# Kernel tuning notes

Measured on AMD Instinct MI355X. Metric: run time of the kernel, lower is better.

## Reference

```python
import jax, jax.numpy as jnp
import numpy as np

D_MODEL = 2048
FFN_MULT = 4
N_ROUTED = 8
TOP_K = 2
H_ROUTED = FFN_MULT * D_MODEL // N_ROUTED   # 1024
H_SHARED = FFN_MULT * D_MODEL               # 8192


def setup_inputs() -> dict:
    key = jax.random.key(0)
    ks = jax.random.split(key, 8)
    s = 0.02
    x = jax.random.normal(ks[0], (4, 2048, D_MODEL), dtype=jnp.float32)
    w_gate = jax.random.normal(ks[1], (N_ROUTED, D_MODEL), dtype=jnp.float32) * s
    Wg = jax.random.normal(ks[2], (N_ROUTED, D_MODEL, H_ROUTED), dtype=jnp.float32) * s
    Wu = jax.random.normal(ks[3], (N_ROUTED, D_MODEL, H_ROUTED), dtype=jnp.float32) * s
    Wd = jax.random.normal(ks[4], (N_ROUTED, H_ROUTED, D_MODEL), dtype=jnp.float32) * s
    Sg = jax.random.normal(ks[5], (D_MODEL, H_SHARED), dtype=jnp.float32) * s
    Su = jax.random.normal(ks[6], (D_MODEL, H_SHARED), dtype=jnp.float32) * s
    Sd = jax.random.normal(ks[7], (H_SHARED, D_MODEL), dtype=jnp.float32) * s
    return {"x": x, "w_gate": w_gate, "Wg": Wg, "Wu": Wu, "Wd": Wd,
            "Sg": Sg, "Su": Su, "Sd": Sd}


def reference(x, w_gate, Wg, Wu, Wd, Sg, Su, Sd):
    B, T, D = x.shape
    N = B * T
    xf = x.reshape(N, D)

    # shared expert (n_shared = 1)
    shared = (jax.nn.silu(xf @ Sg) * (xf @ Su)) @ Sd          # [N, D]

    # gate (eval mode: clean logits, no noise)
    clean = xf @ w_gate.T                                      # [N, E]
    top_logits, top_idx = jax.lax.top_k(clean, TOP_K)          # [N, K]
    gates = jax.nn.softmax(top_logits, axis=-1)                # [N, K]
    # load-balance loss
    importance = jax.nn.softmax(clean, axis=-1).sum(0)         # [E]
    ce = importance / N * N_ROUTED
    lb_loss = jnp.mean(ce * ce)

    # combine weights: combine[n,e] = sum_k gates[n,k] * (top_idx[n,k]==e)
    onehot = jax.nn.one_hot(top_idx, N_ROUTED, dtype=xf.dtype)  # [N, K, E]
    combine = jnp.einsum('nke,nk->ne', onehot, gates)           # [N, E]

    # routed experts (dense grouped form, zero-weight tokens contribute 0)
    hg = jnp.einsum('nd,edh->neh', xf, Wg)
    hu = jnp.einsum('nd,edh->neh', xf, Wu)
    h = jax.nn.silu(hg) * hu                                    # [N, E, H]
    routed = jnp.einsum('neh,ehd,ne->nd', h, Wd, combine)       # [N, D]

    out = (shared + routed).reshape(B, T, D)
    return out, lb_loss
```

## Files before the change

### kernel.cpp

```cpp
#include <hip/hip_runtime.h>
#include <hip/hip_bf16.h>
#include <hip/hip_fp16.h>
#include <stdint.h>

#define NTOK   8192
#define DM     2048
#define NEXP   8
#define HR     1024
#define HS     8192
#define ROWS_MAX 18432

typedef _Float16 f16;
typedef f16  f16x8 __attribute__((ext_vector_type(8)));
typedef float f32x4 __attribute__((ext_vector_type(4)));

#define GLP(p) ((const __attribute__((address_space(1))) void*)(p))
#define LDP(p) ((__attribute__((address_space(3))) void*)(p))

static __device__ __forceinline__ float silu_f(float v) {
  return v / (1.0f + __expf(-v));
}

static __device__ __forceinline__ int xcd_swz(int bid, int nwg) {
  const int q = nwg >> 3, r = nwg & 7;
  const int x = bid & 7, i = bid >> 3;
  return (x < r ? x * (q + 1) : r * (q + 1) + (x - r) * q) + i;
}


__global__ __launch_bounds__(256)
void conv_x_kernel(const float* __restrict__ in, f16* __restrict__ out, int n8) {
  const int i = blockIdx.x * 256 + threadIdx.x;
  if (i >= n8) return;
  const float4* p = (const float4*)in + (size_t)i * 2;
  const float4 a = p[0], b = p[1];
  f16x8 o;
  o[0] = (f16)a.x; o[1] = (f16)a.y; o[2] = (f16)a.z; o[3] = (f16)a.w;
  o[4] = (f16)b.x; o[5] = (f16)b.y; o[6] = (f16)b.z; o[7] = (f16)b.w;
  ((f16x8*)out)[i] = o;
}

__global__ __launch_bounds__(256)
void conv_t_kernel(const float* __restrict__ in, f16* __restrict__ out,
                   int R, int C, size_t ostride) {
  __shared__ float t[32][33];
  const int b = blockIdx.z;
  const float* inb = in + (size_t)b * R * C;
  f16* outb = out + (size_t)b * ostride;
  const int c0 = blockIdx.x * 32, r0 = blockIdx.y * 32;
  const int tx = threadIdx.x, ty0 = threadIdx.y;
#pragma unroll
  for (int yy = 0; yy < 4; ++yy) {
    const int ty = ty0 + yy * 8;
    t[ty][tx] = inb[(size_t)(r0 + ty) * C + (c0 + tx)];
  }
  __syncthreads();
#pragma unroll
  for (int yy = 0; yy < 4; ++yy) {
    const int ty = ty0 + yy * 8;
    outb[(size_t)(c0 + ty) * R + (r0 + tx)] = (f16)t[tx][ty];
  }
}


__global__ __launch_bounds__(256)
void gate_kernel(const float* __restrict__ x, const float* __restrict__ wgate,
                 float* __restrict__ gateW, int* __restrict__ gateI,
                 float* __restrict__ importance, int* __restrict__ cnt) {
  __shared__ float impl[NEXP];
  __shared__ int cntl[NEXP];
  const int tid = threadIdx.x, lane = tid & 63, wid = tid >> 6;
  if (tid < NEXP) { impl[tid] = 0.f; cntl[tid] = 0; }
  __syncthreads();
  for (int s = 0; s < 8; ++s) {
    const int t = blockIdx.x * 32 + wid * 8 + s;
    const float* xr = x + (size_t)t * DM;
    float pv[NEXP] = {0.f, 0.f, 0.f, 0.f, 0.f, 0.f, 0.f, 0.f};
    for (int j = 0; j < DM / 64; ++j) {
      const int c = lane + j * 64;
      const float xv = xr[c];
#pragma unroll
      for (int e = 0; e < NEXP; ++e) pv[e] += xv * wgate[e * DM + c];
    }
#pragma unroll
    for (int e = 0; e < NEXP; ++e) {
#pragma unroll
      for (int st = 32; st >= 1; st >>= 1) pv[e] += __shfl_xor(pv[e], st);
    }
    if (lane == 0) {
      float v1 = pv[0]; int i1 = 0;
#pragma unroll
      for (int e = 1; e < NEXP; ++e) if (pv[e] > v1) { v1 = pv[e]; i1 = e; }
      float v2 = -1e30f; int i2 = 0;
#pragma unroll
      for (int e = 0; e < NEXP; ++e) if (e != i1 && pv[e] > v2) { v2 = pv[e]; i2 = e; }
      const float g1 = 1.f / (1.f + expf(v2 - v1));
      gateW[t * 2 + 0] = g1;  gateW[t * 2 + 1] = 1.f - g1;
      gateI[t * 2 + 0] = i1;  gateI[t * 2 + 1] = i2;
      float mx = pv[0];
#pragma unroll
      for (int e = 1; e < NEXP; ++e) mx = fmaxf(mx, pv[e]);
      float sum = 0.f, ex[NEXP];
#pragma unroll
      for (int e = 0; e < NEXP; ++e) { ex[e] = expf(pv[e] - mx); sum += ex[e]; }
      const float inv = 1.f / sum;
#pragma unroll
      for (int e = 0; e < NEXP; ++e) atomicAdd(&impl[e], ex[e] * inv);
      atomicAdd(&cntl[i1], 1);
      atomicAdd(&cntl[i2], 1);
    }
  }
  __syncthreads();
  if (tid < NEXP) {
    atomicAdd(&importance[tid], impl[tid]);
    atomicAdd(&cnt[tid], cntl[tid]);
  }
}

__global__ void scan_kernel(const int* __restrict__ cnt, int* __restrict__ seg,
                            int* __restrict__ cursor, const float* __restrict__ imp,
                            float* __restrict__ lb_out) {
  if (threadIdx.x == 0 && blockIdx.x == 0) {
    int o = 0;
#pragma unroll
    for (int e = 0; e < NEXP; ++e) {
      seg[e] = o;
      o += (cnt[e] + 255) & ~255;
      cursor[e] = 0;
    }
    seg[NEXP] = o;
    float s = 0.f;
#pragma unroll
    for (int e = 0; e < NEXP; ++e) {
      const float ce = imp[e] * ((float)NEXP / (float)NTOK);
      s += ce * ce;
    }
    *lb_out = s / (float)NEXP;
  }
}

__global__ __launch_bounds__(256)
void scatter_kernel(const float* __restrict__ gateW, const int* __restrict__ gateI,
                    const int* __restrict__ seg, int* __restrict__ cursor,
                    int* __restrict__ rowtok, float* __restrict__ rowgate) {
  const int t = blockIdx.x * 256 + threadIdx.x;
  const int lane = threadIdx.x & 63;
#pragma unroll
  for (int k = 0; k < 2; ++k) {
    const int e = gateI[t * 2 + k];
    const float g = gateW[t * 2 + k];
    for (int ee = 0; ee < NEXP; ++ee) {
      const unsigned long long m = __ballot(e == ee);
      if (e == ee) {
        const int leader = __ffsll((unsigned long long)m) - 1;
        const int rank = (int)__popcll(m & ((1ull << lane) - 1ull));
        int base = 0;
        if (lane == leader) base = atomicAdd(&cursor[ee], (int)__popcll(m));
        base = __shfl(base, leader);
        const int pos = seg[ee] + base + rank;
        rowtok[pos] = t;
        rowgate[pos] = g;
      }
    }
  }
}


struct G8Ptrs { const f16* a[4]; const f16* b[4]; };

static __device__ __forceinline__ void swz_rc(int tid, int i, int& r, int& c) {
  const int L = i * 8192 + tid * 16;
  const int U = L ^ (((L >> 7) & 7) << 4);
  r = U >> 7;
  c = (U & 127) >> 1;
}

static __device__ __forceinline__ void stage8(const G8Ptrs& P, int koff,
                                              f16* AsB, f16* BsB, int wid) {
#pragma unroll
  for (int i = 0; i < 4; ++i) {
    __builtin_amdgcn_global_load_lds(GLP(P.a[i] + koff), LDP(AsB + i * 4096 + wid * 512), 16, 0, 0);
    __builtin_amdgcn_global_load_lds(GLP(P.b[i] + koff), LDP(BsB + i * 4096 + wid * 512), 16, 0, 0);
  }
}

static __device__ __forceinline__ void g8_mainloop(const G8Ptrs& P, int nt,
                                                   f16* As, f16* Bs,
                                                   f32x4 (&acc)[8][4]) {
  const int tid = threadIdx.x;
  const int lane = tid & 63, wid = tid >> 6;
  const int wr = wid >> 2, wc = wid & 3;
  const int fr = lane & 15, fk = (lane >> 4) * 8;

  stage8(P, 0, As, Bs, wid);
  asm volatile("s_waitcnt vmcnt(0)" ::: "memory");
  __syncthreads();

  for (int t = 0; t < nt; ++t) {
    const int cur = t & 1;
    if (t + 1 < nt)
      stage8(P, (t + 1) * 64, As + (cur ^ 1) * 16384, Bs + (cur ^ 1) * 16384, wid);
    const f16* Ab = As + cur * 16384;
    const f16* Bb = Bs + cur * 16384;
    f16x8 bf[4][2];
#pragma unroll
    for (int n = 0; n < 4; ++n) {
      const int r = wc * 64 + n * 16 + fr;
      const int sw = (r & 7) << 3;
#pragma unroll
      for (int ks = 0; ks < 2; ++ks)
        bf[n][ks] = *(const f16x8*)&Bb[(r * 64 + ks * 32 + fk) ^ sw];
    }
#pragma unroll
    for (int mh = 0; mh < 2; ++mh) {
#pragma unroll
      for (int ks = 0; ks < 2; ++ks) {
        f16x8 af[4];
#pragma unroll
        for (int m = 0; m < 4; ++m) {
          const int r = wr * 128 + (mh * 4 + m) * 16 + fr;
          af[m] = *(const f16x8*)&Ab[(r * 64 + ks * 32 + fk) ^ ((r & 7) << 3)];
        }
#pragma unroll
        for (int m = 0; m < 4; ++m)
#pragma unroll
          for (int n = 0; n < 4; ++n)
            acc[mh * 4 + m][n] =
                __builtin_amdgcn_mfma_f32_16x16x32_f16(af[m], bf[n][ks], acc[mh * 4 + m][n], 0, 0, 0);
      }
    }
    asm volatile("s_waitcnt vmcnt(0)" ::: "memory");
    __syncthreads();
  }
}

__global__ __launch_bounds__(512, 2)
void g8_gu(const f16* __restrict__ A, const f16* __restrict__ B,
           f16* __restrict__ C, int gx, int N, int K) {
  __shared__ f16 As[2 * 16384], Bs[2 * 16384];
  const int lin = xcd_swz(blockIdx.x, gridDim.x);
  const int row0 = (lin % gx) * 256, n0 = (lin / gx) * 256;
  const int tid = threadIdx.x;
  G8Ptrs P;
#pragma unroll
  for (int i = 0; i < 4; ++i) {
    int r, c; swz_rc(tid, i, r, c);
    P.a[i] = A + (size_t)(row0 + r) * K + c;
    P.b[i] = B + (size_t)(n0 + r) * K + c;
  }
  f32x4 acc[8][4] = {};
  g8_mainloop(P, K / 64, As, Bs, acc);
  const int lane = tid & 63, wid = tid >> 6;
  const int wr = wid >> 2, wc = wid & 3;
  const int fr = lane & 15, r0 = (lane >> 4) * 4;
#pragma unroll
  for (int m = 0; m < 8; ++m)
#pragma unroll
    for (int n = 0; n < 4; ++n)
#pragma unroll
      for (int rr = 0; rr < 4; ++rr) {
        const int row = row0 + wr * 128 + m * 16 + r0 + rr;
        const int col = n0 + wc * 64 + n * 16 + fr;
        C[(size_t)row * N + col] = (f16)acc[m][n][rr];
      }
}

__global__ __launch_bounds__(512, 2)
void g8_down(const f16* __restrict__ A, const f16* __restrict__ B,
             float* __restrict__ out, int gx, int N, int K, int kchunk) {
  __shared__ f16 As[2 * 16384], Bs[2 * 16384];
  const int lin = xcd_swz(blockIdx.x, gridDim.x);
  const int row0 = (lin % gx) * 256, n0 = (lin / gx) * 256;
  const int k0 = blockIdx.y * kchunk;
  const int tid = threadIdx.x;
  G8Ptrs P;
#pragma unroll
  for (int i = 0; i < 4; ++i) {
    int r, c; swz_rc(tid, i, r, c);
    P.a[i] = A + (size_t)(row0 + r) * K + k0 + c;
    P.b[i] = B + (size_t)(n0 + r) * K + k0 + c;
  }
  f32x4 acc[8][4] = {};
  g8_mainloop(P, kchunk / 64, As, Bs, acc);
  const int lane = tid & 63, wid = tid >> 6;
  const int wr = wid >> 2, wc = wid & 3;
  const int fr = lane & 15, r0 = (lane >> 4) * 4;
#pragma unroll
  for (int m = 0; m < 8; ++m)
#pragma unroll
    for (int n = 0; n < 4; ++n)
#pragma unroll
      for (int rr = 0; rr < 4; ++rr) {
        const int row = row0 + wr * 128 + m * 16 + r0 + rr;
        const int col = n0 + wc * 64 + n * 16 + fr;
        atomicAdd(&out[(size_t)row * N + col], acc[m][n][rr]);
      }
}

__global__ __launch_bounds__(512, 2)
void g8_rgu(const f16* __restrict__ x16, const int* __restrict__ rowtok,
            const f16* __restrict__ Wgu, f16* __restrict__ C,
            const int* __restrict__ seg) {
  __shared__ f16 As[2 * 16384], Bs[2 * 16384];
  const int e = blockIdx.z;
  const int row0 = seg[e] + blockIdx.y * 256;
  if (row0 >= seg[e + 1]) return;
  const int n0 = blockIdx.x * 256;
  const f16* Bbase = Wgu + (size_t)e * 2048 * DM;
  const int tid = threadIdx.x;
  G8Ptrs P;
#pragma unroll
  for (int i = 0; i < 4; ++i) {
    int r, c; swz_rc(tid, i, r, c);
    int tok = rowtok[row0 + r];
    if (tok < 0) tok = 0;
    P.a[i] = x16 + (size_t)tok * DM + c;
    P.b[i] = Bbase + (size_t)(n0 + r) * DM + c;
  }
  f32x4 acc[8][4] = {};
  g8_mainloop(P, DM / 64, As, Bs, acc);
  const int lane = tid & 63, wid = tid >> 6;
  const int wr = wid >> 2, wc = wid & 3;
  const int fr = lane & 15, r0 = (lane >> 4) * 4;
#pragma unroll
  for (int m = 0; m < 8; ++m)
#pragma unroll
    for (int n = 0; n < 4; ++n)
#pragma unroll
      for (int rr = 0; rr < 4; ++rr) {
        const int row = row0 + wr * 128 + m * 16 + r0 + rr;
        const int col = n0 + wc * 64 + n * 16 + fr;
        C[(size_t)row * 2048 + col] = (f16)acc[m][n][rr];
      }
}

__global__ __launch_bounds__(512, 2)
void g8_rdown(const f16* __restrict__ A, const f16* __restrict__ B,
              float* __restrict__ out, const int* __restrict__ seg,
              const int* __restrict__ rowtok, const float* __restrict__ rowgate) {
  __shared__ f16 As[2 * 16384], Bs[2 * 16384];
  const int e = blockIdx.z;
  const int row0 = seg[e] + blockIdx.y * 256;
  if (row0 >= seg[e + 1]) return;
  const int n0 = blockIdx.x * 256;
  const f16* Bbase = B + (size_t)e * DM * HR;
  const int tid = threadIdx.x;
  G8Ptrs P;
#pragma unroll
  for (int i = 0; i < 4; ++i) {
    int r, c; swz_rc(tid, i, r, c);
    P.a[i] = A + (size_t)(row0 + r) * HR + c;
    P.b[i] = Bbase + (size_t)(n0 + r) * HR + c;
  }
  f32x4 acc[8][4] = {};
  g8_mainloop(P, HR / 64, As, Bs, acc);
  const int lane = tid & 63, wid = tid >> 6;
  const int wr = wid >> 2, wc = wid & 3;
  const int fr = lane & 15, r0 = (lane >> 4) * 4;
#pragma unroll
  for (int m = 0; m < 8; ++m)
#pragma unroll
    for (int rr = 0; rr < 4; ++rr) {
      const int pos = row0 + wr * 128 + m * 16 + r0 + rr;
      const int tok = rowtok[pos];
      if (tok >= 0) {
        const float gw = rowgate[pos];
#pragma unroll
        for (int n = 0; n < 4; ++n) {
          const int col = n0 + wc * 64 + n * 16 + fr;
          atomicAdd(&out[(size_t)tok * DM + col], acc[m][n][rr] * gw);
        }
      }
    }
}


__global__ __launch_bounds__(256)
void silu_shared_kernel(const f16* __restrict__ gu, f16* __restrict__ h) {
  const int idx = blockIdx.x * 256 + threadIdx.x;
  const int r = idx >> 10, c8 = idx & 1023;
  const f16x8 g8 = ((const f16x8*)(gu + (size_t)r * 16384))[c8];
  const f16x8 u8 = ((const f16x8*)(gu + (size_t)r * 16384 + 8192))[c8];
  f16x8 o;
#pragma unroll
  for (int j = 0; j < 8; ++j)
    o[j] = (f16)(silu_f((float)g8[j]) * (float)u8[j]);
  ((f16x8*)(h + (size_t)r * 8192))[c8] = o;
}

__global__ __launch_bounds__(256)
void silu_routed_kernel(const f16* __restrict__ gu, f16* __restrict__ hr) {
  const int idx = blockIdx.x * 256 + threadIdx.x;
  const int r = idx >> 7, c8 = idx & 127;
  const f16x8 g8 = ((const f16x8*)(gu + (size_t)r * 2048))[c8];
  const f16x8 u8 = ((const f16x8*)(gu + (size_t)r * 2048 + 1024))[c8];
  f16x8 o;
#pragma unroll
  for (int j = 0; j < 8; ++j)
    o[j] = (f16)(silu_f((float)g8[j]) * (float)u8[j]);
  ((f16x8*)(hr + (size_t)r * 1024))[c8] = o;
}


extern "C" void kernel_launch(void* const* d_in, const int* in_sizes, int n_in,
                              void* d_out, int out_size, void* d_ws, size_t ws_size,
                              hipStream_t stream) {
  const float* x  = (const float*)d_in[0];
  const float* wg = (const float*)d_in[1];
  const float* Wg = (const float*)d_in[2];
  const float* Wu = (const float*)d_in[3];
  const float* Wd = (const float*)d_in[4];
  const float* Sg = (const float*)d_in[5];
  const float* Su = (const float*)d_in[6];
  const float* Sd = (const float*)d_in[7];
  float* out = (float*)d_out;

  char* p = (char*)d_ws;
  auto take = [&](size_t b) { char* q = p; p += (b + 255) & ~(size_t)255; return q; };
  float* importance = (float*)take(32);
  int*   cnt        = (int*)take(32);
  int*   cursor     = (int*)take(32);
  int*   seg        = (int*)take(64);
  int*   rowtok     = (int*)take((size_t)ROWS_MAX * 4);
  float* rowgate    = (float*)take((size_t)ROWS_MAX * 4);
  float* gateW      = (float*)take((size_t)NTOK * 2 * 4);
  int*   gateI      = (int*)take((size_t)NTOK * 2 * 4);
  f16* x16   = (f16*)take((size_t)NTOK * DM * 2);
  f16* SguT  = (f16*)take((size_t)2 * HS * DM * 2);
  f16* SdT   = (f16*)take((size_t)DM * HS * 2);
  f16* WguT  = (f16*)take((size_t)NEXP * 2048 * DM * 2);
  f16* WdT   = (f16*)take((size_t)NEXP * DM * HR * 2);
  f16* hbuf  = (f16*)take((size_t)4096 * HS * 2);
  f16* hr    = (f16*)take((size_t)ROWS_MAX * HR * 2);
  f16* gubuf = (f16*)take((size_t)ROWS_MAX * 2048 * 2);
  if ((size_t)(p - (char*)d_ws) > ws_size) return;

  hipMemsetAsync(out, 0, (size_t)out_size * 4, stream);
  hipMemsetAsync(importance, 0, 768, stream);
  hipMemsetAsync(rowtok, 0xFF, (size_t)ROWS_MAX * 4, stream);

  conv_x_kernel<<<(NTOK * DM / 8 + 255) / 256, 256, 0, stream>>>(x, x16, NTOK * DM / 8);
  dim3 tb(32, 8);
  conv_t_kernel<<<dim3(HS / 32, DM / 32, 1), tb, 0, stream>>>(Sg, SguT, DM, HS, 0);
  conv_t_kernel<<<dim3(HS / 32, DM / 32, 1), tb, 0, stream>>>(Su, SguT + (size_t)HS * DM, DM, HS, 0);
  conv_t_kernel<<<dim3(DM / 32, HS / 32, 1), tb, 0, stream>>>(Sd, SdT, HS, DM, 0);
  conv_t_kernel<<<dim3(HR / 32, DM / 32, NEXP), tb, 0, stream>>>(Wg, WguT, DM, HR, (size_t)2048 * DM);
  conv_t_kernel<<<dim3(HR / 32, DM / 32, NEXP), tb, 0, stream>>>(Wu, WguT + (size_t)HR * DM, DM, HR, (size_t)2048 * DM);
  conv_t_kernel<<<dim3(DM / 32, HR / 32, NEXP), tb, 0, stream>>>(Wd, WdT, HR, DM, (size_t)DM * HR);

  gate_kernel<<<NTOK / 32, 256, 0, stream>>>(x, wg, gateW, gateI, importance, cnt);
  scan_kernel<<<1, 64, 0, stream>>>(cnt, seg, cursor, importance, out + (size_t)NTOK * DM);
  scatter_kernel<<<NTOK / 256, 256, 0, stream>>>(gateW, gateI, seg, cursor, rowtok, rowgate);

  g8_rgu<<<dim3(2048 / 256, 64, NEXP), 512, 0, stream>>>(x16, rowtok, WguT, gubuf, seg);
  silu_routed_kernel<<<ROWS_MAX * 128 / 256, 256, 0, stream>>>(gubuf, hr);
  g8_rdown<<<dim3(DM / 256, 64, NEXP), 512, 0, stream>>>(hr, WdT, out, seg, rowtok, rowgate);

  for (int half = 0; half < 2; ++half) {
    for (int c = 0; c < 2; ++c) {
      const f16* Ax = x16 + ((size_t)half * 4096 + (size_t)c * 2048) * DM;
      g8_gu<<<8 * 64, 512, 0, stream>>>(Ax, SguT, gubuf, 8, 2 * HS, DM);
      silu_shared_kernel<<<2048 * 1024 / 256, 256, 0, stream>>>(gubuf, hbuf + (size_t)c * 2048 * HS);
    }
    g8_down<<<dim3(16 * 8, 2), 512, 0, stream>>>(hbuf, SdT, out + (size_t)half * 4096 * DM,
                                                 16, DM, HS, HS / 2);
  }
}
```

Measured before the change: 1.598 ms.

## Interleave LDS fragment loads, async staging and MFMA phases in g8 mainloop

Splits each K-step of the 256x256 grouped GEMM mainloop into four phases. Each phase loads two A fragments, issues one quarter of the next tile's global-to-LDS copies, then runs MFMAs at raised wave priority behind s_barrier and sched_barrier. The aim is to overlap global prefetch and LDS reads with matrix math instead of issuing all loads up front. It adds extra workgroup barriers per iteration and replaces __syncthreads with raw s_barrier, which risks ordering hazards or stalls if the waits are not placed correctly.

```diff
diff --git a/kernel.cpp b/kernel.cpp
--- a/kernel.cpp
+++ b/kernel.cpp
@@ -184,6 +184,45 @@
   }
 }
 
+#define LOAD_BF()                                                              \
+  _Pragma("unroll")                                                            \
+  for (int n = 0; n < 4; ++n) {                                                \
+    const int r = wc * 64 + n * 16 + fr;                                       \
+    const int sw = (r & 7) << 3;                                               \
+    bf[n][0] = *(const f16x8*)&Bb[(r * 64 + fk) ^ sw];                         \
+    bf[n][1] = *(const f16x8*)&Bb[(r * 64 + 32 + fk) ^ sw];                    \
+  }
+
+#define LOAD_AF(P_)                                                            \
+  _Pragma("unroll")                                                            \
+  for (int i = 0; i < 2; ++i) {                                                \
+    const int r = wr * 128 + (2 * (P_) + i) * 16 + fr;                         \
+    const int sw = (r & 7) << 3;                                               \
+    af[i][0] = *(const f16x8*)&Ab[(r * 64 + fk) ^ sw];                         \
+    af[i][1] = *(const f16x8*)&Ab[(r * 64 + 32 + fk) ^ sw];                    \
+  }
+
+#define STAGE_UNIT(U_)                                                         \
+  if (pf) {                                                                    \
+    __builtin_amdgcn_global_load_lds(GLP(P.a[U_] + koff), LDP(An + (U_) * 4096 + wid * 512), 16, 0, 0); \
+    __builtin_amdgcn_global_load_lds(GLP(P.b[U_] + koff), LDP(Bn + (U_) * 4096 + wid * 512), 16, 0, 0); \
+  }
+
+#define PHASE_MFMA(M0_, M1_)                                                   \
+  __builtin_amdgcn_s_barrier();                                                \
+  asm volatile("s_waitcnt lgkmcnt(0)" ::: "memory");                           \
+  __builtin_amdgcn_sched_barrier(0);                                           \
+  __builtin_amdgcn_s_setprio(1);                                               \
+  _Pragma("unroll")                                                            \
+  for (int ks = 0; ks < 2; ++ks) {                                             \
+    _Pragma("unroll")                                                          \
+    for (int n = 0; n < 4; ++n) {                                              \
+      acc[M0_][n] = __builtin_amdgcn_mfma_f32_16x16x32_f16(af[0][ks], bf[n][ks], acc[M0_][n], 0, 0, 0); \
+      acc[M1_][n] = __builtin_amdgcn_mfma_f32_16x16x32_f16(af[1][ks], bf[n][ks], acc[M1_][n], 0, 0, 0); \
+    }                                                                          \
+  }                                                                            \
+  __builtin_amdgcn_s_setprio(0);
+
 static __device__ __forceinline__ void g8_mainloop(const G8Ptrs& P, int nt,
                                                    f16* As, f16* Bs,
                                                    f32x4 (&acc)[8][4]) {
@@ -198,39 +237,32 @@
 
   for (int t = 0; t < nt; ++t) {
     const int cur = t & 1;
-    if (t + 1 < nt)
-      stage8(P, (t + 1) * 64, As + (cur ^ 1) * 16384, Bs + (cur ^ 1) * 16384, wid);
     const f16* Ab = As + cur * 16384;
     const f16* Bb = Bs + cur * 16384;
-    f16x8 bf[4][2];
-#pragma unroll
-    for (int n = 0; n < 4; ++n) {
-      const int r = wc * 64 + n * 16 + fr;
-      const int sw = (r & 7) << 3;
-#pragma unroll
-      for (int ks = 0; ks < 2; ++ks)
-        bf[n][ks] = *(const f16x8*)&Bb[(r * 64 + ks * 32 + fk) ^ sw];
-    }
-#pragma unroll
-    for (int mh = 0; mh < 2; ++mh) {
-#pragma unroll
-      for (int ks = 0; ks < 2; ++ks) {
-        f16x8 af[4];
-#pragma unroll
-        for (int m = 0; m < 4; ++m) {
-          const int r = wr * 128 + (mh * 4 + m) * 16 + fr;
-          af[m] = *(const f16x8*)&Ab[(r * 64 + ks * 32 + fk) ^ ((r & 7) << 3)];
-        }
-#pragma unroll
-        for (int m = 0; m < 4; ++m)
-#pragma unroll
-          for (int n = 0; n < 4; ++n)
-            acc[mh * 4 + m][n] =
-                __builtin_amdgcn_mfma_f32_16x16x32_f16(af[m], bf[n][ks], acc[mh * 4 + m][n], 0, 0, 0);
-      }
-    }
+    f16* An = As + (cur ^ 1) * 16384;
+    f16* Bn = Bs + (cur ^ 1) * 16384;
+    const int koff = (t + 1) * 64;
+    const bool pf = (t + 1 < nt);
+
+    f16x8 bf[4][2], af[2][2];
+    LOAD_BF();
+    LOAD_AF(0);
+    STAGE_UNIT(0);
+    PHASE_MFMA(0, 1);
+    __builtin_amdgcn_s_barrier();
+    LOAD_AF(1);
+    STAGE_UNIT(1);
+    PHASE_MFMA(2, 3);
+    __builtin_amdgcn_s_barrier();
+    LOAD_AF(2);
+    STAGE_UNIT(2);
+    PHASE_MFMA(4, 5);
+    __builtin_amdgcn_s_barrier();
+    LOAD_AF(3);
+    STAGE_UNIT(3);
+    PHASE_MFMA(6, 7);
     asm volatile("s_waitcnt vmcnt(0)" ::: "memory");
-    __syncthreads();
+    __builtin_amdgcn_s_barrier();
   }
 }
 
```

Result: slower. 1.720 ms (+7.6%).

## Fuse SiLU gating into GEMM epilogues via interleaved gate/up weight layout

Applied to the files above, without the earlier changes.

The gate and up weight columns are interleaved in 16-column groups during the transpose-convert, so each GEMM tile holds matching gate and up accumulators and writes silu(g)*u directly. This removes the separate SiLU kernels and the f16 gate/up intermediate buffer round-trip. The shared path now runs as one full-size up GEMM and one shared down GEMM that stores directly instead of splitting K with atomics, which also drops the output memset. The routed down is then ordered after the shared down so its atomic adds accumulate onto the stored values. In exchange the shared hidden buffer doubles to cover all tokens, and each epilogue writes half as many but more scattered f16 values.

```diff
diff --git a/kernel.cpp b/kernel.cpp
--- a/kernel.cpp
+++ b/kernel.cpp
@@ -42,7 +42,7 @@
 
 __global__ __launch_bounds__(256)
 void conv_t_kernel(const float* __restrict__ in, f16* __restrict__ out,
-                   int R, int C, size_t ostride) {
+                   int R, int C, size_t ostride, int rmap) {
   __shared__ float t[32][33];
   const int b = blockIdx.z;
   const float* inb = in + (size_t)b * R * C;
@@ -58,7 +58,9 @@
 #pragma unroll
   for (int yy = 0; yy < 4; ++yy) {
     const int ty = ty0 + yy * 8;
-    outb[(size_t)(c0 + ty) * R + (r0 + tx)] = (f16)t[tx][ty];
+    const int tr = c0 + ty;
+    const int pr = rmap ? (((tr >> 4) << 5) + ((rmap - 1) << 4) + (tr & 15)) : tr;
+    outb[(size_t)pr * R + (r0 + tx)] = (f16)t[tx][ty];
   }
 }
 
@@ -236,7 +238,7 @@
 
 __global__ __launch_bounds__(512, 2)
 void g8_gu(const f16* __restrict__ A, const f16* __restrict__ B,
-           f16* __restrict__ C, int gx, int N, int K) {
+           f16* __restrict__ H, int gx, int Nh, int K) {
   __shared__ f16 As[2 * 16384], Bs[2 * 16384];
   const int lin = xcd_swz(blockIdx.x, gridDim.x);
   const int row0 = (lin % gx) * 256, n0 = (lin / gx) * 256;
@@ -253,6 +255,40 @@
   const int lane = tid & 63, wid = tid >> 6;
   const int wr = wid >> 2, wc = wid & 3;
   const int fr = lane & 15, r0 = (lane >> 4) * 4;
+  const int hc0 = (n0 + wc * 64) >> 1;
+#pragma unroll
+  for (int m = 0; m < 8; ++m)
+#pragma unroll
+    for (int k = 0; k < 2; ++k)
+#pragma unroll
+      for (int rr = 0; rr < 4; ++rr) {
+        const int row = row0 + wr * 128 + m * 16 + r0 + rr;
+        const int hcol = hc0 + k * 16 + fr;
+        const float g = acc[m][2 * k][rr];
+        const float u = acc[m][2 * k + 1][rr];
+        H[(size_t)row * Nh + hcol] = (f16)(silu_f(g) * u);
+      }
+}
+
+__global__ __launch_bounds__(512, 2)
+void g8_down(const f16* __restrict__ A, const f16* __restrict__ B,
+             float* __restrict__ out, int gx, int N, int K) {
+  __shared__ f16 As[2 * 16384], Bs[2 * 16384];
+  const int lin = xcd_swz(blockIdx.x, gridDim.x);
+  const int row0 = (lin % gx) * 256, n0 = (lin / gx) * 256;
+  const int tid = threadIdx.x;
+  G8Ptrs P;
+#pragma unroll
+  for (int i = 0; i < 4; ++i) {
+    int r, c; swz_rc(tid, i, r, c);
+    P.a[i] = A + (size_t)(row0 + r) * K + c;
+    P.b[i] = B + (size_t)(n0 + r) * K + c;
+  }
+  f32x4 acc[8][4] = {};
+  g8_mainloop(P, K / 64, As, Bs, acc);
+  const int lane = tid & 63, wid = tid >> 6;
+  const int wr = wid >> 2, wc = wid & 3;
+  const int fr = lane & 15, r0 = (lane >> 4) * 4;
 #pragma unroll
   for (int m = 0; m < 8; ++m)
 #pragma unroll
@@ -261,45 +297,13 @@
       for (int rr = 0; rr < 4; ++rr) {
         const int row = row0 + wr * 128 + m * 16 + r0 + rr;
         const int col = n0 + wc * 64 + n * 16 + fr;
-        C[(size_t)row * N + col] = (f16)acc[m][n][rr];
-      }
-}
-
-__global__ __launch_bounds__(512, 2)
-void g8_down(const f16* __restrict__ A, const f16* __restrict__ B,
-             float* __restrict__ out, int gx, int N, int K, int kchunk) {
-  __shared__ f16 As[2 * 16384], Bs[2 * 16384];
-  const int lin = xcd_swz(blockIdx.x, gridDim.x);
-  const int row0 = (lin % gx) * 256, n0 = (lin / gx) * 256;
-  const int k0 = blockIdx.y * kchunk;
-  const int tid = threadIdx.x;
-  G8Ptrs P;
-#pragma unroll
-  for (int i = 0; i < 4; ++i) {
-    int r, c; swz_rc(tid, i, r, c);
-    P.a[i] = A + (size_t)(row0 + r) * K + k0 + c;
-    P.b[i] = B + (size_t)(n0 + r) * K + k0 + c;
-  }
-  f32x4 acc[8][4] = {};
-  g8_mainloop(P, kchunk / 64, As, Bs, acc);
-  const int lane = tid & 63, wid = tid >> 6;
-  const int wr = wid >> 2, wc = wid & 3;
-  const int fr = lane & 15, r0 = (lane >> 4) * 4;
-#pragma unroll
-  for (int m = 0; m < 8; ++m)
-#pragma unroll
-    for (int n = 0; n < 4; ++n)
-#pragma unroll
-      for (int rr = 0; rr < 4; ++rr) {
-        const int row = row0 + wr * 128 + m * 16 + r0 + rr;
-        const int col = n0 + wc * 64 + n * 16 + fr;
-        atomicAdd(&out[(size_t)row * N + col], acc[m][n][rr]);
+        out[(size_t)row * N + col] = acc[m][n][rr];
       }
 }
 
 __global__ __launch_bounds__(512, 2)
 void g8_rgu(const f16* __restrict__ x16, const int* __restrict__ rowtok,
-            const f16* __restrict__ Wgu, f16* __restrict__ C,
+            const f16* __restrict__ Wgu, f16* __restrict__ hr,
             const int* __restrict__ seg) {
   __shared__ f16 As[2 * 16384], Bs[2 * 16384];
   const int e = blockIdx.z;
@@ -322,15 +326,18 @@
   const int lane = tid & 63, wid = tid >> 6;
   const int wr = wid >> 2, wc = wid & 3;
   const int fr = lane & 15, r0 = (lane >> 4) * 4;
+  const int hc0 = (n0 + wc * 64) >> 1;
 #pragma unroll
   for (int m = 0; m < 8; ++m)
 #pragma unroll
-    for (int n = 0; n < 4; ++n)
+    for (int k = 0; k < 2; ++k)
 #pragma unroll
       for (int rr = 0; rr < 4; ++rr) {
         const int row = row0 + wr * 128 + m * 16 + r0 + rr;
-        const int col = n0 + wc * 64 + n * 16 + fr;
-        C[(size_t)row * 2048 + col] = (f16)acc[m][n][rr];
+        const int hcol = hc0 + k * 16 + fr;
+        const float g = acc[m][2 * k][rr];
+        const float u = acc[m][2 * k + 1][rr];
+        hr[(size_t)row * HR + hcol] = (f16)(silu_f(g) * u);
       }
 }
 
@@ -375,33 +382,6 @@
 }
 
 
-__global__ __launch_bounds__(256)
-void silu_shared_kernel(const f16* __restrict__ gu, f16* __restrict__ h) {
-  const int idx = blockIdx.x * 256 + threadIdx.x;
-  const int r = idx >> 10, c8 = idx & 1023;
-  const f16x8 g8 = ((const f16x8*)(gu + (size_t)r * 16384))[c8];
-  const f16x8 u8 = ((const f16x8*)(gu + (size_t)r * 16384 + 8192))[c8];
-  f16x8 o;
-#pragma unroll
-  for (int j = 0; j < 8; ++j)
-    o[j] = (f16)(silu_f((float)g8[j]) * (float)u8[j]);
-  ((f16x8*)(h + (size_t)r * 8192))[c8] = o;
-}
-
-__global__ __launch_bounds__(256)
-void silu_routed_kernel(const f16* __restrict__ gu, f16* __restrict__ hr) {
-  const int idx = blockIdx.x * 256 + threadIdx.x;
-  const int r = idx >> 7, c8 = idx & 127;
-  const f16x8 g8 = ((const f16x8*)(gu + (size_t)r * 2048))[c8];
-  const f16x8 u8 = ((const f16x8*)(gu + (size_t)r * 2048 + 1024))[c8];
-  f16x8 o;
-#pragma unroll
-  for (int j = 0; j < 8; ++j)
-    o[j] = (f16)(silu_f((float)g8[j]) * (float)u8[j]);
-  ((f16x8*)(hr + (size_t)r * 1024))[c8] = o;
-}
-
-
 extern "C" void kernel_launch(void* const* d_in, const int* in_sizes, int n_in,
                               void* d_out, int out_size, void* d_ws, size_t ws_size,
                               hipStream_t stream) {
@@ -426,43 +406,34 @@
   float* gateW      = (float*)take((size_t)NTOK * 2 * 4);
   int*   gateI      = (int*)take((size_t)NTOK * 2 * 4);
   f16* x16   = (f16*)take((size_t)NTOK * DM * 2);
-  f16* SguT  = (f16*)take((size_t)2 * HS * DM * 2);
+  f16* SguI  = (f16*)take((size_t)2 * HS * DM * 2);
   f16* SdT   = (f16*)take((size_t)DM * HS * 2);
-  f16* WguT  = (f16*)take((size_t)NEXP * 2048 * DM * 2);
+  f16* WguI  = (f16*)take((size_t)NEXP * 2048 * DM * 2);
   f16* WdT   = (f16*)take((size_t)NEXP * DM * HR * 2);
-  f16* hbuf  = (f16*)take((size_t)4096 * HS * 2);
+  f16* hbuf  = (f16*)take((size_t)NTOK * HS * 2);
   f16* hr    = (f16*)take((size_t)ROWS_MAX * HR * 2);
-  f16* gubuf = (f16*)take((size_t)ROWS_MAX * 2048 * 2);
   if ((size_t)(p - (char*)d_ws) > ws_size) return;
 
-  hipMemsetAsync(out, 0, (size_t)out_size * 4, stream);
   hipMemsetAsync(importance, 0, 768, stream);
   hipMemsetAsync(rowtok, 0xFF, (size_t)ROWS_MAX * 4, stream);
 
   conv_x_kernel<<<(NTOK * DM / 8 + 255) / 256, 256, 0, stream>>>(x, x16, NTOK * DM / 8);
   dim3 tb(32, 8);
-  conv_t_kernel<<<dim3(HS / 32, DM / 32, 1), tb, 0, stream>>>(Sg, SguT, DM, HS, 0);
-  conv_t_kernel<<<dim3(HS / 32, DM / 32, 1), tb, 0, stream>>>(Su, SguT + (size_t)HS * DM, DM, HS, 0);
-  conv_t_kernel<<<dim3(DM / 32, HS / 32, 1), tb, 0, stream>>>(Sd, SdT, HS, DM, 0);
-  conv_t_kernel<<<dim3(HR / 32, DM / 32, NEXP), tb, 0, stream>>>(Wg, WguT, DM, HR, (size_t)2048 * DM);
-  conv_t_kernel<<<dim3(HR / 32, DM / 32, NEXP), tb, 0, stream>>>(Wu, WguT + (size_t)HR * DM, DM, HR, (size_t)2048 * DM);
-  conv_t_kernel<<<dim3(DM / 32, HR / 32, NEXP), tb, 0, stream>>>(Wd, WdT, HR, DM, (size_t)DM * HR);
+  conv_t_kernel<<<dim3(HS / 32, DM / 32, 1), tb, 0, stream>>>(Sg, SguI, DM, HS, 0, 1);
+  conv_t_kernel<<<dim3(HS / 32, DM / 32, 1), tb, 0, stream>>>(Su, SguI, DM, HS, 0, 2);
+  conv_t_kernel<<<dim3(DM / 32, HS / 32, 1), tb, 0, stream>>>(Sd, SdT, HS, DM, 0, 0);
+  conv_t_kernel<<<dim3(HR / 32, DM / 32, NEXP), tb, 0, stream>>>(Wg, WguI, DM, HR, (size_t)2048 * DM, 1);
+  conv_t_kernel<<<dim3(HR / 32, DM / 32, NEXP), tb, 0, stream>>>(Wu, WguI, DM, HR, (size_t)2048 * DM, 2);
+  conv_t_kernel<<<dim3(DM / 32, HR / 32, NEXP), tb, 0, stream>>>(Wd, WdT, HR, DM, (size_t)DM * HR, 0);
 
   gate_kernel<<<NTOK / 32, 256, 0, stream>>>(x, wg, gateW, gateI, importance, cnt);
   scan_kernel<<<1, 64, 0, stream>>>(cnt, seg, cursor, importance, out + (size_t)NTOK * DM);
   scatter_kernel<<<NTOK / 256, 256, 0, stream>>>(gateW, gateI, seg, cursor, rowtok, rowgate);
 
-  g8_rgu<<<dim3(2048 / 256, 64, NEXP), 512, 0, stream>>>(x16, rowtok, WguT, gubuf, seg);
-  silu_routed_kernel<<<ROWS_MAX * 128 / 256, 256, 0, stream>>>(gubuf, hr);
-  g8_rdown<<<dim3(DM / 256, 64, NEXP), 512, 0, stream>>>(hr, WdT, out, seg, rowtok, rowgate);
-
-  for (int half = 0; half < 2; ++half) {
-    for (int c = 0; c < 2; ++c) {
-      const f16* Ax = x16 + ((size_t)half * 4096 + (size_t)c * 2048) * DM;
-      g8_gu<<<8 * 64, 512, 0, stream>>>(Ax, SguT, gubuf, 8, 2 * HS, DM);
-      silu_shared_kernel<<<2048 * 1024 / 256, 256, 0, stream>>>(gubuf, hbuf + (size_t)c * 2048 * HS);
-    }
-    g8_down<<<dim3(16 * 8, 2), 512, 0, stream>>>(hbuf, SdT, out + (size_t)half * 4096 * DM,
-                                                 16, DM, HS, HS / 2);
-  }
-}
+  g8_rgu<<<dim3(8, 64, NEXP), 512, 0, stream>>>(x16, rowtok, WguI, hr, seg);
+
+  g8_gu<<<32 * 64, 512, 0, stream>>>(x16, SguI, hbuf, 32, HS, DM);
+  g8_down<<<32 * 8, 512, 0, stream>>>(hbuf, SdT, out, 32, DM, HS);
+
+  g8_rdown<<<dim3(8, 64, NEXP), 512, 0, stream>>>(hr, WdT, out, seg, rowtok, rowgate);
+}
```

New measurement: 1.447 ms. 9.5% less time.
